# Optimization experiments

Hardware: AMD Instinct MI355X
Metric: run time of the kernel (lower is better)

Reference implementation:

```python
import jax, jax.numpy as jnp
import numpy as np

EPS = 1e-6
MIN_EIG = 1e-4
TAU = 1.0  # obs_temperature


def _expm(A):
    """Batched matrix exponential for small KxK matrices via scaling-and-squaring
    + 12-term Taylor (matches torch.linalg.matrix_exp to ~1e-6 for moderate norms).
    Fully differentiable in both modes. A: (..., K, K)."""
    s = 6
    A = A * (1.0 / 2.0 ** s)
    I = jnp.eye(A.shape[-1], dtype=A.dtype)
    E = I + A
    term = A
    for k in range(2, 13):
        term = jnp.matmul(term, A) / k
        E = E + term
    for _ in range(s):
        E = jnp.matmul(E, E)
    return E


def setup_inputs() -> dict:
    key = jax.random.key(0)
    ks = jax.random.split(key, 6)
    B, N, K, V = 1, 2048, 3, 8192
    I = jnp.eye(K, dtype=jnp.float32)
    Ap = jax.random.normal(ks[0], (B, N, K, K), jnp.float32)
    Sigma_prior = Ap @ jnp.swapaxes(Ap, -1, -2) / K + 0.5 * I  # SPD
    Aq = jax.random.normal(ks[1], (B, N, K, K), jnp.float32)
    Sigma_q = Aq @ jnp.swapaxes(Aq, -1, -2) / K + 0.5 * I  # SPD
    phi = 0.5 * jax.random.normal(ks[2], (B, N, 3), jnp.float32)
    beta = jax.nn.softmax(jax.random.normal(ks[3], (B, N, N), jnp.float32), axis=-1)
    mu = jax.random.normal(ks[4], (B, N, K), jnp.float32)
    W_out = jax.random.normal(ks[5], (V, K), jnp.float32) / jnp.sqrt(float(K))
    generators = jnp.array([[[0, 0, 0], [0, 0, -1], [0, 1, 0]],
                            [[0, 0, 1], [0, 0, 0], [-1, 0, 0]],
                            [[0, -1, 0], [1, 0, 0], [0, 0, 0]]], jnp.float32)
    return dict(Sigma_prior=Sigma_prior, Sigma_q=Sigma_q, phi=phi, beta=beta,
                mu=mu, W_out=W_out, generators=generators)


def reference(Sigma_prior, Sigma_q, phi, beta, mu, W_out, generators):
    B, N, K = mu.shape
    dt = Sigma_prior.dtype
    I = jnp.eye(K, dtype=dt)

    # Prior precision Lambda_p = (Sigma_p + eps I)^{-1}
    Lambda_p = jnp.linalg.inv(Sigma_prior + EPS * I)

    # Categorical observation precision: Lambda_o = Cov_p(W) / tau^2
    logits = jnp.einsum('bnk,vk->bnv', mu, W_out) / TAU
    p = jax.nn.softmax(logits, axis=-1)                                # (B,N,V)
    mean_w = jnp.einsum('bnv,vk->bnk', p, W_out)                        # E_p[w]
    second = jnp.einsum('bnv,vk,vl->bnkl', p, W_out, W_out)             # E_p[ww^T]
    Lambda_o = (second - jnp.einsum('bnk,bnl->bnkl', mean_w, mean_w)) / TAU ** 2
    Lambda_o = 0.5 * (Lambda_o + jnp.swapaxes(Lambda_o, -1, -2)) + EPS * I

    # Posterior precision
    Lambda_q = jnp.linalg.inv(Sigma_q + EPS * I)                        # (B,N,K,K)

    # Gauge transport Omega_{ij} = e^{phi_i} e^{-phi_j}
    phi_mat = jnp.einsum('bnc,ckl->bnkl', phi, generators)              # (B,N,K,K)
    exp_phi = _expm(phi_mat)
    exp_neg_phi = _expm(-phi_mat)
    Omega = jnp.einsum('bikl,bjlm->bijkm', exp_phi, exp_neg_phi)        # (B,N,N,K,K)

    # Transported precision Lambda~_{qj in i-frame} = Omega Lambda_q Omega^T
    Lt = jnp.einsum('bijkl,bjlm,bijnm->bijkn', Omega, Lambda_q, Omega)  # (B,N,N,K,K)
    M_incoming = jnp.einsum('bij,bijkn->bikn', beta, Lt)                # (B,N,K,K)

    # Outgoing recoil: (sum_j beta_{ji}) * Lambda_{qi}
    M_outgoing = beta.sum(axis=1)[..., None, None] * Lambda_q

    M = Lambda_p + Lambda_o + M_incoming + M_outgoing
    M = 0.5 * (M + jnp.swapaxes(M, -1, -2))
    bad = ~jnp.isfinite(M)
    M = jnp.where(bad, jnp.broadcast_to(I, M.shape), M)
    M = M + max(MIN_EIG, 1e-4) * I

    # Eigenvalue floor and inverse
    w, v = jnp.linalg.eigh(M.astype(jnp.float32))
    w = jnp.clip(w, MIN_EIG, None)
    M_pd = jnp.einsum('...ij,...j,...kj->...ik', v, w, v)
    M_inv = jnp.einsum('...ij,...j,...kj->...ik', v, 1.0 / w, v)
    return M_pd.astype(dt), M_inv.astype(dt)
```

## Files before the change

kernel.cpp:

```cpp
#include <hip/hip_runtime.h>
#include <math.h>

#define EPSV 1e-6f
#define MINEIG 1e-4f


__device__ __forceinline__ void mm3(const float a[3][3], const float b[3][3], float c[3][3]) {
#pragma unroll
  for (int i = 0; i < 3; ++i)
#pragma unroll
    for (int j = 0; j < 3; ++j)
      c[i][j] = fmaf(a[i][0], b[0][j], fmaf(a[i][1], b[1][j], a[i][2] * b[2][j]));
}

__device__ __forceinline__ void inv3(const float a[3][3], float inv[3][3]) {
  float c00 = a[1][1] * a[2][2] - a[1][2] * a[2][1];
  float c01 = -(a[1][0] * a[2][2] - a[1][2] * a[2][0]);
  float c02 = a[1][0] * a[2][1] - a[1][1] * a[2][0];
  float det = a[0][0] * c00 + a[0][1] * c01 + a[0][2] * c02;
  float id = 1.0f / det;
  inv[0][0] = c00 * id;
  inv[0][1] = (a[0][2] * a[2][1] - a[0][1] * a[2][2]) * id;
  inv[0][2] = (a[0][1] * a[1][2] - a[0][2] * a[1][1]) * id;
  inv[1][0] = c01 * id;
  inv[1][1] = (a[0][0] * a[2][2] - a[0][2] * a[2][0]) * id;
  inv[1][2] = (a[0][2] * a[1][0] - a[0][0] * a[1][2]) * id;
  inv[2][0] = c02 * id;
  inv[2][1] = (a[0][1] * a[2][0] - a[0][0] * a[2][1]) * id;
  inv[2][2] = (a[0][0] * a[1][1] - a[0][1] * a[1][0]) * id;
}

__device__ void expm3(const float A[3][3], float E[3][3]) {
  float As[3][3], term[3][3], tmp[3][3];
#pragma unroll
  for (int i = 0; i < 3; ++i)
#pragma unroll
    for (int j = 0; j < 3; ++j) {
      As[i][j] = A[i][j] * (1.0f / 64.0f);
      term[i][j] = As[i][j];
      E[i][j] = ((i == j) ? 1.0f : 0.0f) + As[i][j];
    }
  for (int k = 2; k <= 12; ++k) {
    mm3(term, As, tmp);
    float r = 1.0f / (float)k;
#pragma unroll
    for (int i = 0; i < 3; ++i)
#pragma unroll
      for (int j = 0; j < 3; ++j) {
        term[i][j] = tmp[i][j] * r;
        E[i][j] += term[i][j];
      }
  }
  for (int s = 0; s < 6; ++s) {
    mm3(E, E, tmp);
#pragma unroll
    for (int i = 0; i < 3; ++i)
#pragma unroll
      for (int j = 0; j < 3; ++j) E[i][j] = tmp[i][j];
  }
}

template <int P, int Q, int RI>
__device__ __forceinline__ void jrot(float A[3][3], float V[3][3]) {
  float apq = A[P][Q];
  if (fabsf(apq) < 1e-20f) return;
  float theta = (A[Q][Q] - A[P][P]) / (2.0f * apq);
  float t = copysignf(1.0f, theta) / (fabsf(theta) + sqrtf(fmaf(theta, theta, 1.0f)));
  float c = 1.0f / sqrtf(fmaf(t, t, 1.0f));
  float s = t * c;
  A[P][P] = A[P][P] - t * apq;
  A[Q][Q] = A[Q][Q] + t * apq;
  A[P][Q] = 0.f; A[Q][P] = 0.f;
  float arp = A[RI][P], arq = A[RI][Q];
  float nrp = c * arp - s * arq;
  float nrq = s * arp + c * arq;
  A[RI][P] = nrp; A[P][RI] = nrp;
  A[RI][Q] = nrq; A[Q][RI] = nrq;
#pragma unroll
  for (int i = 0; i < 3; ++i) {
    float vip = V[i][P], viq = V[i][Q];
    V[i][P] = c * vip - s * viq;
    V[i][Q] = s * vip + c * viq;
  }
}

__device__ __forceinline__ bool finitef(float x) {
  return !(isnan(x) || isinf(x));
}


__global__ void stageA_kernel(const float* __restrict__ Sp, const float* __restrict__ Sq,
                              const float* __restrict__ phi, const float* __restrict__ gen,
                              const float* __restrict__ beta, const float* __restrict__ mu,
                              const float* __restrict__ W,
                              float* __restrict__ Lp, float* __restrict__ Lq,
                              float* __restrict__ Rm, float* __restrict__ Ssoa,
                              float* __restrict__ pcs, float* __restrict__ Lo,
                              int N, int V) {
  int bid = blockIdx.x;
  int tid = threadIdx.x;
  int nPrep = N >> 8;
  int nCT = N >> 8;
  int nColsum = (N >> 5) * nCT;
  if (bid < nPrep) {
    int i = bid * 256 + tid;
    float a[3][3], lp[3][3], lq[3][3];
#pragma unroll
    for (int k = 0; k < 3; ++k)
#pragma unroll
      for (int l = 0; l < 3; ++l)
        a[k][l] = Sp[i * 9 + k * 3 + l] + ((k == l) ? EPSV : 0.0f);
    inv3(a, lp);
#pragma unroll
    for (int k = 0; k < 3; ++k)
#pragma unroll
      for (int l = 0; l < 3; ++l)
        a[k][l] = Sq[i * 9 + k * 3 + l] + ((k == l) ? EPSV : 0.0f);
    inv3(a, lq);

    float p0 = phi[i * 3 + 0], p1 = phi[i * 3 + 1], p2 = phi[i * 3 + 2];
    float A[3][3];
#pragma unroll
    for (int k = 0; k < 3; ++k)
#pragma unroll
      for (int l = 0; l < 3; ++l)
        A[k][l] = p0 * gen[0 + k * 3 + l] + p1 * gen[9 + k * 3 + l] + p2 * gen[18 + k * 3 + l];
    float R[3][3];
    expm3(A, R);
    float Rt[3][3];
#pragma unroll
    for (int k = 0; k < 3; ++k)
#pragma unroll
      for (int l = 0; l < 3; ++l) Rt[k][l] = R[l][k];
    float t1[3][3], S[3][3];
    mm3(lq, R, t1);
    mm3(Rt, t1, S);
#pragma unroll
    for (int k = 0; k < 3; ++k)
#pragma unroll
      for (int l = 0; l < 3; ++l) {
        Lp[i * 9 + k * 3 + l] = lp[k][l];
        Lq[i * 9 + k * 3 + l] = lq[k][l];
        Rm[i * 9 + k * 3 + l] = R[k][l];
        Ssoa[(k * 3 + l) * N + i] = S[k][l];
      }
  } else if (bid < nPrep + nColsum) {
    int cb = bid - nPrep;
    int rs = cb / nCT;
    int ct = cb % nCT;
    int j = ct * 256 + tid;
    const float* bp = beta + (size_t)(rs * 32) * N + j;
    float s = 0.f;
#pragma unroll
    for (int r = 0; r < 32; ++r) s += bp[(size_t)r * N];
    pcs[(size_t)rs * N + j] = s;
  } else {
    int n0 = (bid - nPrep - nColsum) * 4;
    float m[4][3];
#pragma unroll
    for (int j = 0; j < 4; ++j) {
      m[j][0] = mu[(n0 + j) * 3 + 0];
      m[j][1] = mu[(n0 + j) * 3 + 1];
      m[j][2] = mu[(n0 + j) * 3 + 2];
    }
    float acc[4][10];
#pragma unroll
    for (int j = 0; j < 4; ++j)
#pragma unroll
      for (int k = 0; k < 10; ++k) acc[j][k] = 0.f;

    const float4* W4 = (const float4*)W;
    for (int vb = tid; vb * 4 < V; vb += 256) {
      float4 f0 = W4[vb * 3 + 0];
      float4 f1 = W4[vb * 3 + 1];
      float4 f2 = W4[vb * 3 + 2];
      float wv[4][3] = {{f0.x, f0.y, f0.z}, {f0.w, f1.x, f1.y},
                        {f1.z, f1.w, f2.x}, {f2.y, f2.z, f2.w}};
#pragma unroll
      for (int c = 0; c < 4; ++c) {
        float w0 = wv[c][0], w1 = wv[c][1], w2 = wv[c][2];
        float p00 = w0 * w0, p01 = w0 * w1, p02 = w0 * w2;
        float p11 = w1 * w1, p12 = w1 * w2, p22 = w2 * w2;
#pragma unroll
        for (int j = 0; j < 4; ++j) {
          float l = fmaf(m[j][0], w0, fmaf(m[j][1], w1, m[j][2] * w2));
          float e = __expf(l);
          acc[j][0] += e;
          acc[j][1] = fmaf(e, w0, acc[j][1]);
          acc[j][2] = fmaf(e, w1, acc[j][2]);
          acc[j][3] = fmaf(e, w2, acc[j][3]);
          acc[j][4] = fmaf(e, p00, acc[j][4]);
          acc[j][5] = fmaf(e, p01, acc[j][5]);
          acc[j][6] = fmaf(e, p02, acc[j][6]);
          acc[j][7] = fmaf(e, p11, acc[j][7]);
          acc[j][8] = fmaf(e, p12, acc[j][8]);
          acc[j][9] = fmaf(e, p22, acc[j][9]);
        }
      }
    }

    __shared__ float sred[4][40];
#pragma unroll
    for (int j = 0; j < 4; ++j)
#pragma unroll
      for (int k = 0; k < 10; ++k) {
        float x = acc[j][k];
#pragma unroll
        for (int o = 32; o > 0; o >>= 1) x += __shfl_down(x, o, 64);
        if ((tid & 63) == 0) sred[tid >> 6][j * 10 + k] = x;
      }
    __syncthreads();
    if (tid < 4) {
      int j = tid;
      float tot[10];
#pragma unroll
      for (int k = 0; k < 10; ++k)
        tot[k] = sred[0][j * 10 + k] + sred[1][j * 10 + k] +
                 sred[2][j * 10 + k] + sred[3][j * 10 + k];
      float inv = 1.0f / tot[0];
      float mw0 = tot[1] * inv, mw1 = tot[2] * inv, mw2 = tot[3] * inv;
      float* o = Lo + (n0 + j) * 9;
      o[0] = tot[4] * inv - mw0 * mw0 + EPSV;
      float v01 = tot[5] * inv - mw0 * mw1;
      float v02 = tot[6] * inv - mw0 * mw2;
      o[1] = v01; o[3] = v01;
      o[2] = v02; o[6] = v02;
      o[4] = tot[7] * inv - mw1 * mw1 + EPSV;
      float v12 = tot[8] * inv - mw1 * mw2;
      o[5] = v12; o[7] = v12;
      o[8] = tot[9] * inv - mw2 * mw2 + EPSV;
    }
  }
}


__global__ void bmm_fold_kernel(const float* __restrict__ beta, const float* __restrict__ Ssoa,
                                const float* __restrict__ pcs, float* __restrict__ T,
                                float* __restrict__ cs, int N) {
  int lane = threadIdx.x & 63;
  int w = threadIdx.x >> 6;
  int nRow = N >> 2;
  if ((int)blockIdx.x < nRow) {
    int i = blockIdx.x * 4 + w;
    const float4* B4 = (const float4*)(beta + (size_t)i * N);
    float acc[9];
#pragma unroll
    for (int k = 0; k < 9; ++k) acc[k] = 0.f;

    for (int jt = 0; jt < N; jt += 256) {
      int q = (jt >> 2) + lane;
      float4 b = B4[q];
      float4 sv[9];
#pragma unroll
      for (int k = 0; k < 9; ++k) sv[k] = ((const float4*)(Ssoa + k * N))[q];
#pragma unroll
      for (int k = 0; k < 9; ++k) {
        acc[k] = fmaf(b.x, sv[k].x, acc[k]);
        acc[k] = fmaf(b.y, sv[k].y, acc[k]);
        acc[k] = fmaf(b.z, sv[k].z, acc[k]);
        acc[k] = fmaf(b.w, sv[k].w, acc[k]);
      }
    }
#pragma unroll
    for (int k = 0; k < 9; ++k) {
      float x = acc[k];
#pragma unroll
      for (int o = 32; o > 0; o >>= 1) x += __shfl_down(x, o, 64);
      if (lane == 0) T[i * 9 + k] = x;
    }
  } else {
    int n = (blockIdx.x - nRow) * 4 + w;
    int RS = N >> 5;
    float x = 0.f;
    for (int r = lane; r < RS; r += 64) x += pcs[(size_t)r * N + n];
#pragma unroll
    for (int o = 32; o > 0; o >>= 1) x += __shfl_down(x, o, 64);
    if (lane == 0) cs[n] = x;
  }
}


__global__ void finalize_kernel(const float* __restrict__ Lp, const float* __restrict__ Lq,
                                const float* __restrict__ Rm, const float* __restrict__ Lo,
                                const float* __restrict__ T, const float* __restrict__ cs,
                                float* __restrict__ out, int N) {
  int i = blockIdx.x * blockDim.x + threadIdx.x;
  if (i >= N) return;

  float c = cs[i];
  float R[3][3], Tm[3][3], M[3][3];
#pragma unroll
  for (int k = 0; k < 3; ++k)
#pragma unroll
    for (int l = 0; l < 3; ++l) {
      R[k][l] = Rm[i * 9 + k * 3 + l];
      Tm[k][l] = T[i * 9 + k * 3 + l];
    }
  float t1[3][3], Rt[3][3], Min[3][3];
  mm3(R, Tm, t1);
#pragma unroll
  for (int k = 0; k < 3; ++k)
#pragma unroll
    for (int l = 0; l < 3; ++l) Rt[k][l] = R[l][k];
  mm3(t1, Rt, Min);
#pragma unroll
  for (int k = 0; k < 3; ++k)
#pragma unroll
    for (int l = 0; l < 3; ++l)
      M[k][l] = Lp[i * 9 + k * 3 + l] + Lo[i * 9 + k * 3 + l] + Min[k][l] +
                c * Lq[i * 9 + k * 3 + l];
#pragma unroll
  for (int k = 0; k < 3; ++k)
#pragma unroll
    for (int l = 0; l < 3; ++l) {
      if (l > k) {
        float v = 0.5f * (M[k][l] + M[l][k]);
        M[k][l] = v; M[l][k] = v;
      }
    }
#pragma unroll
  for (int k = 0; k < 3; ++k)
#pragma unroll
    for (int l = 0; l < 3; ++l)
      if (!finitef(M[k][l])) M[k][l] = (k == l) ? 1.0f : 0.0f;
  M[0][0] += MINEIG; M[1][1] += MINEIG; M[2][2] += MINEIG;

  float A[3][3], Vv[3][3] = {{1, 0, 0}, {0, 1, 0}, {0, 0, 1}};
#pragma unroll
  for (int k = 0; k < 3; ++k)
#pragma unroll
    for (int l = 0; l < 3; ++l) A[k][l] = M[k][l];
  for (int sweep = 0; sweep < 8; ++sweep) {
    jrot<0, 1, 2>(A, Vv);
    jrot<0, 2, 1>(A, Vv);
    jrot<1, 2, 0>(A, Vv);
  }
  float wc[3], wi[3];
#pragma unroll
  for (int k = 0; k < 3; ++k) {
    wc[k] = fmaxf(A[k][k], MINEIG);
    wi[k] = 1.0f / wc[k];
  }
#pragma unroll
  for (int k = 0; k < 3; ++k)
#pragma unroll
    for (int l = 0; l < 3; ++l) {
      float mpd = Vv[k][0] * wc[0] * Vv[l][0] + Vv[k][1] * wc[1] * Vv[l][1] +
                  Vv[k][2] * wc[2] * Vv[l][2];
      float mnv = Vv[k][0] * wi[0] * Vv[l][0] + Vv[k][1] * wi[1] * Vv[l][1] +
                  Vv[k][2] * wi[2] * Vv[l][2];
      out[i * 9 + k * 3 + l] = mpd;
      out[(size_t)N * 9 + i * 9 + k * 3 + l] = mnv;
    }
}


extern "C" void kernel_launch(void* const* d_in, const int* in_sizes, int n_in,
                              void* d_out, int out_size, void* d_ws, size_t ws_size,
                              hipStream_t stream) {
  const float* Sp = (const float*)d_in[0];
  const float* Sq = (const float*)d_in[1];
  const float* phi = (const float*)d_in[2];
  const float* beta = (const float*)d_in[3];
  const float* mu = (const float*)d_in[4];
  const float* W = (const float*)d_in[5];
  const float* gen = (const float*)d_in[6];
  float* out = (float*)d_out;

  const int N = in_sizes[2] / 3;
  const int V = in_sizes[5] / 3;

  float* ws = (float*)d_ws;
  float* Lp = ws;
  float* Lq = Lp + (size_t)N * 9;
  float* Rm = Lq + (size_t)N * 9;
  float* Ssoa = Rm + (size_t)N * 9;
  float* Lo = Ssoa + (size_t)N * 9;
  float* T = Lo + (size_t)N * 9;
  float* pcs = T + (size_t)N * 9;
  float* cs = pcs + (size_t)(N / 32) * N;

  int nPrep = N / 256;
  int nColsum = (N / 32) * (N / 256);
  int nLo = N / 4;
  stageA_kernel<<<nPrep + nColsum + nLo, 256, 0, stream>>>(
      Sp, Sq, phi, gen, beta, mu, W, Lp, Lq, Rm, Ssoa, pcs, Lo, N, V);
  bmm_fold_kernel<<<N / 4 + N / 4, 256, 0, stream>>>(beta, Ssoa, pcs, T, cs, N);
  finalize_kernel<<<N / 64, 64, 0, stream>>>(Lp, Lq, Rm, Lo, T, cs, out, N);
}
```

Measured before the change: 112.9 us.

## Fuse beta-weighted fold, column-sum reduction and finalize into one kernel

Merges the row-wise beta·S reduction, the column-sum reduction and the per-token eigen-finalize into a single kernel, one wavefront per row. Each wave broadcasts the reduced 3x3 and column sum to all lanes, runs the Jacobi eigensolver redundantly on every lane, and lets lanes 0-8 write the outputs. This removes a kernel launch and the global round trip through the T and cs buffers. In exchange, the column-sum read assumes exactly 64 partial rows (N/32 == 64), and every lane repeats the eigen work.

```diff
diff --git a/kernel.cpp b/kernel.cpp
--- a/kernel.cpp
+++ b/kernel.cpp
@@ -234,67 +234,58 @@
 }
 
 
-__global__ void bmm_fold_kernel(const float* __restrict__ beta, const float* __restrict__ Ssoa,
-                                const float* __restrict__ pcs, float* __restrict__ T,
-                                float* __restrict__ cs, int N) {
+__global__ void bmm_finalize_kernel(const float* __restrict__ beta,
+                                    const float* __restrict__ Ssoa,
+                                    const float* __restrict__ pcs,
+                                    const float* __restrict__ Lp,
+                                    const float* __restrict__ Lq,
+                                    const float* __restrict__ Rm,
+                                    const float* __restrict__ Lo,
+                                    float* __restrict__ out, int N) {
   int lane = threadIdx.x & 63;
   int w = threadIdx.x >> 6;
-  int nRow = N >> 2;
-  if ((int)blockIdx.x < nRow) {
-    int i = blockIdx.x * 4 + w;
-    const float4* B4 = (const float4*)(beta + (size_t)i * N);
-    float acc[9];
-#pragma unroll
-    for (int k = 0; k < 9; ++k) acc[k] = 0.f;
-
-    for (int jt = 0; jt < N; jt += 256) {
-      int q = (jt >> 2) + lane;
-      float4 b = B4[q];
-      float4 sv[9];
-#pragma unroll
-      for (int k = 0; k < 9; ++k) sv[k] = ((const float4*)(Ssoa + k * N))[q];
-#pragma unroll
-      for (int k = 0; k < 9; ++k) {
-        acc[k] = fmaf(b.x, sv[k].x, acc[k]);
-        acc[k] = fmaf(b.y, sv[k].y, acc[k]);
-        acc[k] = fmaf(b.z, sv[k].z, acc[k]);
-        acc[k] = fmaf(b.w, sv[k].w, acc[k]);
-      }
-    }
+  int i = blockIdx.x * 4 + w;
+
+  const float4* B4 = (const float4*)(beta + (size_t)i * N);
+  float acc[9];
+#pragma unroll
+  for (int k = 0; k < 9; ++k) acc[k] = 0.f;
+
+  for (int jt = 0; jt < N; jt += 256) {
+    int q = (jt >> 2) + lane;
+    float4 b = B4[q];
+    float4 sv[9];
+#pragma unroll
+    for (int k = 0; k < 9; ++k) sv[k] = ((const float4*)(Ssoa + k * N))[q];
 #pragma unroll
     for (int k = 0; k < 9; ++k) {
-      float x = acc[k];
-#pragma unroll
-      for (int o = 32; o > 0; o >>= 1) x += __shfl_down(x, o, 64);
-      if (lane == 0) T[i * 9 + k] = x;
-    }
-  } else {
-    int n = (blockIdx.x - nRow) * 4 + w;
-    int RS = N >> 5;
-    float x = 0.f;
-    for (int r = lane; r < RS; r += 64) x += pcs[(size_t)r * N + n];
+      acc[k] = fmaf(b.x, sv[k].x, acc[k]);
+      acc[k] = fmaf(b.y, sv[k].y, acc[k]);
+      acc[k] = fmaf(b.z, sv[k].z, acc[k]);
+      acc[k] = fmaf(b.w, sv[k].w, acc[k]);
+    }
+  }
+  float tv[9];
+#pragma unroll
+  for (int k = 0; k < 9; ++k) {
+    float x = acc[k];
 #pragma unroll
     for (int o = 32; o > 0; o >>= 1) x += __shfl_down(x, o, 64);
-    if (lane == 0) cs[n] = x;
-  }
-}
-
-
-__global__ void finalize_kernel(const float* __restrict__ Lp, const float* __restrict__ Lq,
-                                const float* __restrict__ Rm, const float* __restrict__ Lo,
-                                const float* __restrict__ T, const float* __restrict__ cs,
-                                float* __restrict__ out, int N) {
-  int i = blockIdx.x * blockDim.x + threadIdx.x;
-  if (i >= N) return;
-
-  float c = cs[i];
+    tv[k] = __shfl(x, 0, 64);
+  }
+
+  float cc = pcs[(size_t)lane * N + i];
+#pragma unroll
+  for (int o = 32; o > 0; o >>= 1) cc += __shfl_down(cc, o, 64);
+  float c = __shfl(cc, 0, 64);
+
   float R[3][3], Tm[3][3], M[3][3];
 #pragma unroll
   for (int k = 0; k < 3; ++k)
 #pragma unroll
     for (int l = 0; l < 3; ++l) {
       R[k][l] = Rm[i * 9 + k * 3 + l];
-      Tm[k][l] = T[i * 9 + k * 3 + l];
+      Tm[k][l] = tv[k * 3 + l];
     }
   float t1[3][3], Rt[3][3], Min[3][3];
   mm3(R, Tm, t1);
@@ -341,17 +332,15 @@
     wc[k] = fmaxf(A[k][k], MINEIG);
     wi[k] = 1.0f / wc[k];
   }
-#pragma unroll
-  for (int k = 0; k < 3; ++k)
-#pragma unroll
-    for (int l = 0; l < 3; ++l) {
-      float mpd = Vv[k][0] * wc[0] * Vv[l][0] + Vv[k][1] * wc[1] * Vv[l][1] +
-                  Vv[k][2] * wc[2] * Vv[l][2];
-      float mnv = Vv[k][0] * wi[0] * Vv[l][0] + Vv[k][1] * wi[1] * Vv[l][1] +
-                  Vv[k][2] * wi[2] * Vv[l][2];
-      out[i * 9 + k * 3 + l] = mpd;
-      out[(size_t)N * 9 + i * 9 + k * 3 + l] = mnv;
-    }
+  if (lane < 9) {
+    int k = lane / 3, l = lane % 3;
+    float mpd = Vv[k][0] * wc[0] * Vv[l][0] + Vv[k][1] * wc[1] * Vv[l][1] +
+                Vv[k][2] * wc[2] * Vv[l][2];
+    float mnv = Vv[k][0] * wi[0] * Vv[l][0] + Vv[k][1] * wi[1] * Vv[l][1] +
+                Vv[k][2] * wi[2] * Vv[l][2];
+    out[i * 9 + lane] = mpd;
+    out[(size_t)N * 9 + i * 9 + lane] = mnv;
+  }
 }
 
 
@@ -376,15 +365,12 @@
   float* Rm = Lq + (size_t)N * 9;
   float* Ssoa = Rm + (size_t)N * 9;
   float* Lo = Ssoa + (size_t)N * 9;
-  float* T = Lo + (size_t)N * 9;
-  float* pcs = T + (size_t)N * 9;
-  float* cs = pcs + (size_t)(N / 32) * N;
+  float* pcs = Lo + (size_t)N * 9;
 
   int nPrep = N / 256;
   int nColsum = (N / 32) * (N / 256);
   int nLo = N / 4;
   stageA_kernel<<<nPrep + nColsum + nLo, 256, 0, stream>>>(
       Sp, Sq, phi, gen, beta, mu, W, Lp, Lq, Rm, Ssoa, pcs, Lo, N, V);
-  bmm_fold_kernel<<<N / 4 + N / 4, 256, 0, stream>>>(beta, Ssoa, pcs, T, cs, N);
-  finalize_kernel<<<N / 64, 64, 0, stream>>>(Lp, Lq, Rm, Lo, T, cs, out, N);
-}
+  bmm_finalize_kernel<<<N / 4, 256, 0, stream>>>(beta, Ssoa, pcs, Lp, Lq, Rm, Lo, out, N);
+}
```

Result: no change. 111.7 us (median of 2 runs) (-1.1%).
